# Kernel tuning notes

Measured on AMD Instinct MI355X. Metric: run time of the kernel, lower is better.

The kernel has to match this reference:

```python
import jax, jax.numpy as jnp
import numpy as np

HEADS = 8

def setup_inputs() -> dict:
    key = jax.random.key(0)
    k1, k2, k3, k4 = jax.random.split(key, 4)
    B, C_IN, H, W = 16, 256, 64, 64
    C_OUT = 256
    s = 1.0 / np.sqrt(C_IN)
    x = jax.random.normal(k1, (B, C_IN, H, W), dtype=jnp.float32)
    wq = jax.random.normal(k2, (C_OUT, C_IN), dtype=jnp.float32) * s
    wk = jax.random.normal(k3, (C_OUT, C_IN), dtype=jnp.float32) * s
    wv = jax.random.normal(k4, (C_OUT, C_IN), dtype=jnp.float32) * s
    return {"x": x, "wq": wq, "wk": wk, "wv": wv}

def _feat(t):
    # ELU(x) + 1  (positive feature map for linear attention)
    return jax.nn.elu(t) + 1.0

def reference(x, wq, wk, wv):
    B, C, H, W = x.shape
    M = H * W
    c_out = wq.shape[0]
    dh = c_out // HEADS
    scale = 1.0 / np.sqrt(dh)
    xf = x.reshape(B, C, M)  # flatten spatial
    # 1x1 conv (no bias) == channel matmul; reshape to [B, heads, dh, M]
    def proj(w):
        return jnp.einsum('oc,bcm->bom', w, xf).reshape(B, HEADS, dh, M)
    q = _feat(proj(wq)) * scale
    k = _feat(proj(wk)) * scale
    v = proj(wv)
    # linear attention: KV = k v^T over spatial, then apply to q
    KV = jnp.einsum('bhcm,bhdm->bhcd', k, v)          # [B,h,dh,dh]
    out = jnp.einsum('bhcd,bhcm->bhdm', KV, q)        # [B,h,dh,M]
    k_sum = k.sum(axis=-1)                             # [B,h,dh]
    denom = jnp.einsum('bhcm,bhc->bhm', q, k_sum)      # [B,h,M]
    denom = jnp.maximum(denom, 1e-6)[:, :, None, :]
    out = out / denom
    return out.reshape(B, c_out, H, W)
```

## Files before the change

### kernel.cpp

```cpp
#include <hip/hip_runtime.h>
#include <hip/hip_bf16.h>


typedef __attribute__((ext_vector_type(8))) short bf16x8;
typedef __attribute__((ext_vector_type(4))) float f32x4;
typedef __attribute__((ext_vector_type(4))) unsigned int u32x4;
typedef __attribute__((ext_vector_type(4))) float float4v;

#define DEVI static __device__ __forceinline__

DEVI unsigned short f2bf(float f){
  unsigned int u = __builtin_bit_cast(unsigned int, f);
  u = (u + 0x7fffu + ((u >> 16) & 1u)) >> 16;
  return (unsigned short)u;
}
DEVI unsigned int pk2(float a, float b){
  return (unsigned int)f2bf(a) | ((unsigned int)f2bf(b) << 16);
}
DEVI float feat(float p){
  return (p > 0.f ? p + 1.f : __expf(p)) * 0.17677669529663687f;
}

DEVI f32x4 mfma16(u32x4 a, u32x4 b, f32x4 c){
  return __builtin_amdgcn_mfma_f32_16x16x32_bf16(
      __builtin_bit_cast(bf16x8, a), __builtin_bit_cast(bf16x8, b), c, 0, 0, 0);
}

DEVI int swz8(int m){ return ((m ^ (m >> 3)) & 7) << 4; }

typedef __attribute__((address_space(3))) unsigned int as3_u32;
typedef __attribute__((address_space(1))) const unsigned int as1_u32;
DEVI void gload16(const void* g, void* l){
  __builtin_amdgcn_global_load_lds((as1_u32*)g, (as3_u32*)l, 16, 0, 0);
}
DEVI void stage_tile(const char* src, void* buf, int w, int lane){
  #pragma unroll
  for (int i = 0; i < 4; ++i){
    int ub = w * 1024 + i * 8192;
    gload16(src + ub + lane * 16, (char*)buf + ub);
  }
}

DEVI void stage_load(const float* __restrict__ xb, int m0, int tid, float4v* r){
  #pragma unroll
  for (int it = 0; it < 2; ++it){
    int cq = (tid >> 4) + it * 32;
    int mq = tid & 15;
    const float* p = xb + (size_t)(cq * 4) * 4096 + m0 + mq * 4;
    r[it*4+0] = *(const float4v*)(p);
    r[it*4+1] = *(const float4v*)(p + 4096);
    r[it*4+2] = *(const float4v*)(p + 8192);
    r[it*4+3] = *(const float4v*)(p + 12288);
  }
}
DEVI void stage_write(unsigned short* xT, int tid, const float4v* r){
  #pragma unroll
  for (int it = 0; it < 2; ++it){
    int cq = (tid >> 4) + it * 32;
    int mq = tid & 15;
    int c0 = cq * 4, ml0 = mq * 4;
    #pragma unroll
    for (int j = 0; j < 4; ++j){
      int m = ml0 + j;
      unsigned int lo = pk2(r[it*4+0][j], r[it*4+1][j]);
      unsigned int hi = pk2(r[it*4+2][j], r[it*4+3][j]);
      int off = m * 512 + ((c0 * 2) ^ swz8(m));
      unsigned long long v = (unsigned long long)lo | ((unsigned long long)hi << 32);
      *(unsigned long long*)((char*)xT + off) = v;
    }
  }
}
DEVI void dump_tile_sw(const unsigned short* xT, unsigned short* dst, int tid){
  #pragma unroll
  for (int i = 0; i < 4; ++i){
    int f = i * 512 + tid;
    int lane = f & 63, nt = (f >> 6) & 3, kk = f >> 8;
    int m = nt * 16 + (lane & 15);
    int col = (kk * 64 + (lane >> 4) * 16) ^ swz8(m);
    u32x4 v = *(const u32x4*)((const char*)xT + m * 512 + col);
    *(u32x4*)((char*)dst + (size_t)f * 16) = v;
  }
}

__global__ void wconv(const float* __restrict__ wq, const float* __restrict__ wk,
                      const float* __restrict__ wv,
                      unsigned short* __restrict__ wkvf, unsigned short* __restrict__ wqf){
  int t = blockIdx.x * 256 + threadIdx.x;
  if (t < 16384){
    int lane = t & 63, kk = (t >> 6) & 7, ot = (t >> 9) & 3, h = t >> 11;
    int l15 = lane & 15, hi = lane >> 4;
    const float* src = (ot < 2) ? (wk + (size_t)(h * 32 + ot * 16 + l15) * 256)
                                : (wv + (size_t)(h * 32 + (ot - 2) * 16 + l15) * 256);
    src += kk * 32 + hi * 8;
    unsigned short* dst = wkvf + (size_t)t * 8;
    #pragma unroll
    for (int j = 0; j < 8; ++j) dst[j] = f2bf(src[j]);
  } else if (t < 24576){
    int u = t - 16384;
    int lane = u & 63, kk = (u >> 6) & 7, ot = (u >> 9) & 1, h = u >> 10;
    int l15 = lane & 15, hi = lane >> 4;
    const float* src = wq + (size_t)(h * 32 + ot * 16 + l15) * 256 + kk * 32 + hi * 8;
    unsigned short* dst = wqf + (size_t)u * 8;
    #pragma unroll
    for (int j = 0; j < 8; ++j) dst[j] = f2bf(src[j]);
  }
}

DEVI void compute_sub_sw(const unsigned short* __restrict__ xT,
                         const unsigned short* __restrict__ wkvf,
                         int w, int l15, int hi, int lane,
                         f32x4 (&kvacc)[2][2], f32x4 (&ksacc)[2], u32x4 ones){
  #pragma unroll
  for (int g = 0; g < 2; ++g){
    f32x4 acc[2][4];
    #pragma unroll
    for (int a1 = 0; a1 < 2; ++a1)
      #pragma unroll
      for (int a2 = 0; a2 < 4; ++a2) acc[a1][a2] = f32x4{0.f,0.f,0.f,0.f};

    #pragma unroll
    for (int kk = 0; kk < 8; ++kk){
      u32x4 xf[2];
      #pragma unroll
      for (int n2 = 0; n2 < 2; ++n2){
        int m = (g * 2 + n2) * 16 + l15;
        xf[n2] = *(const u32x4*)((const char*)xT + m * 512 + ((kk * 64 + hi * 16) ^ swz8(m)));
      }
      #pragma unroll
      for (int ot = 0; ot < 4; ++ot){
        u32x4 wf = *(const u32x4*)(wkvf + ((((size_t)w * 4 + ot) * 8 + kk) * 64 + lane) * 8);
        #pragma unroll
        for (int n2 = 0; n2 < 2; ++n2) acc[n2][ot] = mfma16(xf[n2], wf, acc[n2][ot]);
      }
    }
    u32x4 kf[2], vf[2];
    #pragma unroll
    for (int t2 = 0; t2 < 2; ++t2){
      kf[t2][0] = pk2(feat(acc[0][t2][0]), feat(acc[0][t2][1]));
      kf[t2][1] = pk2(feat(acc[0][t2][2]), feat(acc[0][t2][3]));
      kf[t2][2] = pk2(feat(acc[1][t2][0]), feat(acc[1][t2][1]));
      kf[t2][3] = pk2(feat(acc[1][t2][2]), feat(acc[1][t2][3]));
      vf[t2][0] = pk2(acc[0][t2+2][0], acc[0][t2+2][1]);
      vf[t2][1] = pk2(acc[0][t2+2][2], acc[0][t2+2][3]);
      vf[t2][2] = pk2(acc[1][t2+2][0], acc[1][t2+2][1]);
      vf[t2][3] = pk2(acc[1][t2+2][2], acc[1][t2+2][3]);
    }
    #pragma unroll
    for (int ct = 0; ct < 2; ++ct){
      #pragma unroll
      for (int dt = 0; dt < 2; ++dt)
        kvacc[ct][dt] = mfma16(kf[ct], vf[dt], kvacc[ct][dt]);
      ksacc[ct] = mfma16(kf[ct], ones, ksacc[ct]);
    }
  }
}

__global__ void __launch_bounds__(512) xkv(const float* __restrict__ x,
        const unsigned short* __restrict__ wkvf,
        unsigned short* __restrict__ ximg,
        float* __restrict__ kvp, float* __restrict__ ksp){
  __shared__ __align__(16) unsigned short xT[16384];
  const int tid = threadIdx.x, lane = tid & 63, w = tid >> 6;
  const int l15 = lane & 15, hi = lane >> 4;
  const int t = blockIdx.x, b = blockIdx.y;
  const float* xb = x + (size_t)b * (256 * 4096);
  unsigned short* img = ximg + ((size_t)b * 64 + t) * 16384;

  f32x4 kvacc[2][2];
  f32x4 ksacc[2];
  #pragma unroll
  for (int i = 0; i < 2; ++i){
    ksacc[i] = f32x4{0.f,0.f,0.f,0.f};
    #pragma unroll
    for (int j = 0; j < 2; ++j) kvacc[i][j] = f32x4{0.f,0.f,0.f,0.f};
  }
  u32x4 ones = {0u,0u,0u,0u};
  if (l15 == 0){ ones[0] = ones[1] = ones[2] = ones[3] = 0x3f803f80u; }

  {
    float4v rs[8];
    stage_load(xb, t * 64, tid, rs);
    stage_write(xT, tid, rs);
  }
  __syncthreads();
  dump_tile_sw(xT, img, tid);
  compute_sub_sw(xT, wkvf, w, l15, hi, lane, kvacc, ksacc, ones);

  size_t base = (((size_t)b * 64 + t) * 8 + w) * 1024;
  #pragma unroll
  for (int ct = 0; ct < 2; ++ct){
    #pragma unroll
    for (int dt = 0; dt < 2; ++dt){
      #pragma unroll
      for (int r = 0; r < 4; ++r){
        int c = ct * 16 + hi * 4 + r, d = dt * 16 + l15;
        kvp[base + c * 32 + d] = kvacc[ct][dt][r];
      }
    }
  }
  if (l15 == 0){
    size_t kb = (((size_t)b * 64 + t) * 8 + w) * 32;
    #pragma unroll
    for (int ct = 0; ct < 2; ++ct)
      #pragma unroll
      for (int r = 0; r < 4; ++r) ksp[kb + ct * 16 + hi * 4 + r] = ksacc[ct][r];
  }
}

__global__ void k_red(const float* __restrict__ kvp, const float* __restrict__ ksp,
                      unsigned short* __restrict__ kvt, unsigned short* __restrict__ ksb){
  int t = blockIdx.x * 256 + threadIdx.x;
  int dq = t & 7;
  int c  = (t >> 3) & 31;
  int h  = (t >> 8) & 7;
  int b  = t >> 11;
  float4v s = {0.f,0.f,0.f,0.f};
  for (int c2 = 0; c2 < 64; ++c2){
    const float* p = kvp + ((((size_t)b * 64 + c2) * 8 + h) * 1024) + c * 32 + dq * 4;
    float4v r = *(const float4v*)p;
    s.x += r.x; s.y += r.y; s.z += r.z; s.w += r.w;
  }
  int pos = ((c >> 2) & 3) * 8 + ((c >> 4) << 2) + (c & 3);
  unsigned short* q = kvt + ((size_t)b * 8 + h) * 1024;
  q[(dq * 4 + 0) * 32 + pos] = f2bf(s.x);
  q[(dq * 4 + 1) * 32 + pos] = f2bf(s.y);
  q[(dq * 4 + 2) * 32 + pos] = f2bf(s.z);
  q[(dq * 4 + 3) * 32 + pos] = f2bf(s.w);
  if (dq == 0){
    float ks = 0.f;
    for (int c2 = 0; c2 < 64; ++c2)
      ks += ksp[(((size_t)b * 64 + c2) * 8 + h) * 32 + c];
    ksb[((size_t)b * 8 + h) * 32 + pos] = f2bf(ks);
  }
}

DEVI void q_sub(const unsigned short* __restrict__ xT,
                const unsigned short* __restrict__ wqf,
                u32x4 afkv0, u32x4 afkv1, u32x4 afd,
                int w, int l15, int hi, int lane, float* __restrict__ ob){
  f32x4 qa[2][4];
  #pragma unroll
  for (int a1 = 0; a1 < 2; ++a1)
    #pragma unroll
    for (int a2 = 0; a2 < 4; ++a2) qa[a1][a2] = f32x4{0.f,0.f,0.f,0.f};

  #pragma unroll
  for (int kk = 0; kk < 8; ++kk){
    u32x4 xf[4];
    #pragma unroll
    for (int nt = 0; nt < 4; ++nt)
      xf[nt] = *(const u32x4*)(xT + (((size_t)kk * 4 + nt) * 64 + lane) * 8);
    #pragma unroll
    for (int ot = 0; ot < 2; ++ot){
      u32x4 wf = *(const u32x4*)(wqf + ((((size_t)w * 2 + ot) * 8 + kk) * 64 + lane) * 8);
      #pragma unroll
      for (int nt = 0; nt < 4; ++nt) qa[ot][nt] = mfma16(wf, xf[nt], qa[ot][nt]);
    }
  }

  #pragma unroll
  for (int nt = 0; nt < 4; ++nt){
    u32x4 bq;
    bq[0] = pk2(feat(qa[0][nt][0]), feat(qa[0][nt][1]));
    bq[1] = pk2(feat(qa[0][nt][2]), feat(qa[0][nt][3]));
    bq[2] = pk2(feat(qa[1][nt][0]), feat(qa[1][nt][1]));
    bq[3] = pk2(feat(qa[1][nt][2]), feat(qa[1][nt][3]));

    f32x4 o0 = {0.f,0.f,0.f,0.f}, o1 = {0.f,0.f,0.f,0.f}, dn = {0.f,0.f,0.f,0.f};
    o0 = mfma16(afkv0, bq, o0);
    o1 = mfma16(afkv1, bq, o1);
    dn = mfma16(afd, bq, dn);
    float dv = __shfl(dn[0], l15, 64);
    float inv = 1.0f / fmaxf(dv, 1e-6f);
    #pragma unroll
    for (int r = 0; r < 4; ++r){
      ob[(size_t)(hi * 4 + r) * 4096 + nt * 16 + l15]      = o0[r] * inv;
      ob[(size_t)(16 + hi * 4 + r) * 4096 + nt * 16 + l15] = o1[r] * inv;
    }
  }
}

__global__ void __launch_bounds__(512) k_q(const unsigned short* __restrict__ ximg,
        const unsigned short* __restrict__ wqf,
        const unsigned short* __restrict__ kvt,
        const unsigned short* __restrict__ ksb,
        float* __restrict__ out){
  __shared__ __align__(16) unsigned short xT[2][16384];
  const int tid = threadIdx.x, lane = tid & 63, w = tid >> 6;
  const int l15 = lane & 15, hi = lane >> 4;
  const int ch = blockIdx.x, b = blockIdx.y;
  const char* src = (const char*)(ximg + ((size_t)b * 64 + ch * 2) * 16384);

  size_t kvbase = ((size_t)b * 8 + w) * 1024;
  u32x4 afkv0 = *(const u32x4*)(kvt + kvbase + (size_t)l15 * 32 + hi * 8);
  u32x4 afkv1 = *(const u32x4*)(kvt + kvbase + (size_t)(16 + l15) * 32 + hi * 8);
  u32x4 afd = {0u,0u,0u,0u};
  if (l15 == 0) afd = *(const u32x4*)(ksb + ((size_t)b * 8 + w) * 32 + hi * 8);

  stage_tile(src, xT[0], w, lane);
  __syncthreads();
  stage_tile(src + 32768, xT[1], w, lane);

  float* ob = out + ((size_t)b * 256 + w * 32) * 4096 + ch * 128;
  q_sub(xT[0], wqf, afkv0, afkv1, afd, w, l15, hi, lane, ob);
  __syncthreads();
  q_sub(xT[1], wqf, afkv0, afkv1, afd, w, l15, hi, lane, ob + 64);
}

extern "C" void kernel_launch(void* const* d_in, const int* in_sizes, int n_in,
                              void* d_out, int out_size, void* d_ws, size_t ws_size,
                              hipStream_t stream) {
  const float* x  = (const float*)d_in[0];
  const float* wq = (const float*)d_in[1];
  const float* wk = (const float*)d_in[2];
  const float* wv = (const float*)d_in[3];
  float* out = (float*)d_out;
  char* ws = (char*)d_ws;

  unsigned short* wkvf = (unsigned short*)(ws);
  unsigned short* wqf  = (unsigned short*)(ws + 262144);
  unsigned short* kvt  = (unsigned short*)(ws + 393216);
  unsigned short* ksb  = (unsigned short*)(ws + 655360);
  float* kvp = (float*)(ws + 1048576);
  float* ksp = (float*)(ws + 1048576 + 33554432);
  unsigned short* ximg = (unsigned short*)(ws + 1048576 + 33554432 + 1048576);

  hipLaunchKernelGGL(wconv, dim3(96), dim3(256), 0, stream, wq, wk, wv, wkvf, wqf);
  hipLaunchKernelGGL(xkv,   dim3(64, 16), dim3(512), 0, stream, x, wkvf, ximg, kvp, ksp);
  hipLaunchKernelGGL(k_red, dim3(128), dim3(256), 0, stream, kvp, ksp, kvt, ksb);
  hipLaunchKernelGGL(k_q,   dim3(32, 16), dim3(512), 0, stream, ximg, wqf, kvt, ksb, out);
}
```

Before: 80.07 us.

## Double-buffer x tiles in xkv with 1024-thread blocks over two chunks

The xkv kernel now runs 1024 threads per block, and each block handles two 64-column spatial tiles through a two-slot shared buffer. The global load of the second tile is issued before computing on the first, so memory latency can overlap with MFMA work. Each wave now handles one head and one 32-column half of a tile, and the partial-sum indexing is remapped to match. The manual bf16 rounding is also replaced with the library __float2bfloat16. The larger block raises per-block shared memory and register pressure under launch_bounds(1024), and the grid shrinks by half, which may lower occupancy.

```diff
diff --git a/kernel.cpp b/kernel.cpp
--- a/kernel.cpp
+++ b/kernel.cpp
@@ -10,9 +10,8 @@
 #define DEVI static __device__ __forceinline__
 
 DEVI unsigned short f2bf(float f){
-  unsigned int u = __builtin_bit_cast(unsigned int, f);
-  u = (u + 0x7fffu + ((u >> 16) & 1u)) >> 16;
-  return (unsigned short)u;
+  __hip_bfloat16 h = __float2bfloat16(f);
+  return __builtin_bit_cast(unsigned short, h);
 }
 DEVI unsigned int pk2(float a, float b){
   return (unsigned int)f2bf(a) | ((unsigned int)f2bf(b) << 16);
@@ -41,39 +40,33 @@
   }
 }
 
-DEVI void stage_load(const float* __restrict__ xb, int m0, int tid, float4v* r){
-  #pragma unroll
-  for (int it = 0; it < 2; ++it){
-    int cq = (tid >> 4) + it * 32;
-    int mq = tid & 15;
-    const float* p = xb + (size_t)(cq * 4) * 4096 + m0 + mq * 4;
-    r[it*4+0] = *(const float4v*)(p);
-    r[it*4+1] = *(const float4v*)(p + 4096);
-    r[it*4+2] = *(const float4v*)(p + 8192);
-    r[it*4+3] = *(const float4v*)(p + 12288);
-  }
-}
-DEVI void stage_write(unsigned short* xT, int tid, const float4v* r){
-  #pragma unroll
-  for (int it = 0; it < 2; ++it){
-    int cq = (tid >> 4) + it * 32;
-    int mq = tid & 15;
-    int c0 = cq * 4, ml0 = mq * 4;
-    #pragma unroll
-    for (int j = 0; j < 4; ++j){
-      int m = ml0 + j;
-      unsigned int lo = pk2(r[it*4+0][j], r[it*4+1][j]);
-      unsigned int hi = pk2(r[it*4+2][j], r[it*4+3][j]);
-      int off = m * 512 + ((c0 * 2) ^ swz8(m));
-      unsigned long long v = (unsigned long long)lo | ((unsigned long long)hi << 32);
-      *(unsigned long long*)((char*)xT + off) = v;
-    }
-  }
-}
-DEVI void dump_tile_sw(const unsigned short* xT, unsigned short* dst, int tid){
-  #pragma unroll
-  for (int i = 0; i < 4; ++i){
-    int f = i * 512 + tid;
+DEVI void stage_load1k(const float* __restrict__ xb, int m0, int tid, float4v* r){
+  int cq = tid >> 4;
+  int mq = tid & 15;
+  const float* p = xb + (size_t)(cq * 4) * 4096 + m0 + mq * 4;
+  r[0] = *(const float4v*)(p);
+  r[1] = *(const float4v*)(p + 4096);
+  r[2] = *(const float4v*)(p + 8192);
+  r[3] = *(const float4v*)(p + 12288);
+}
+DEVI void stage_write1k(unsigned short* xT, int tid, const float4v* r){
+  int cq = tid >> 4;
+  int mq = tid & 15;
+  int c0 = cq * 4, ml0 = mq * 4;
+  #pragma unroll
+  for (int j = 0; j < 4; ++j){
+    int m = ml0 + j;
+    unsigned int lo = pk2(r[0][j], r[1][j]);
+    unsigned int hi = pk2(r[2][j], r[3][j]);
+    int off = m * 512 + ((c0 * 2) ^ swz8(m));
+    unsigned long long v = (unsigned long long)lo | ((unsigned long long)hi << 32);
+    *(unsigned long long*)((char*)xT + off) = v;
+  }
+}
+DEVI void dump_tile_1k(const unsigned short* xT, unsigned short* dst, int tid){
+  #pragma unroll
+  for (int i = 0; i < 2; ++i){
+    int f = i * 1024 + tid;
     int lane = f & 63, nt = (f >> 6) & 3, kk = f >> 8;
     int m = nt * 16 + (lane & 15);
     int col = (kk * 64 + (lane >> 4) * 16) ^ swz8(m);
@@ -106,65 +99,63 @@
   }
 }
 
-DEVI void compute_sub_sw(const unsigned short* __restrict__ xT,
-                         const unsigned short* __restrict__ wkvf,
-                         int w, int l15, int hi, int lane,
-                         f32x4 (&kvacc)[2][2], f32x4 (&ksacc)[2], u32x4 ones){
-  #pragma unroll
-  for (int g = 0; g < 2; ++g){
-    f32x4 acc[2][4];
-    #pragma unroll
-    for (int a1 = 0; a1 < 2; ++a1)
+DEVI void compute_half_sw(const unsigned short* __restrict__ xT,
+                          const unsigned short* __restrict__ wkvf,
+                          int h, int g, int l15, int hi, int lane,
+                          f32x4 (&kvacc)[2][2], f32x4 (&ksacc)[2], u32x4 ones){
+  f32x4 acc[2][4];
+  #pragma unroll
+  for (int a1 = 0; a1 < 2; ++a1)
+    #pragma unroll
+    for (int a2 = 0; a2 < 4; ++a2) acc[a1][a2] = f32x4{0.f,0.f,0.f,0.f};
+
+  #pragma unroll
+  for (int kk = 0; kk < 8; ++kk){
+    u32x4 xf[2];
+    #pragma unroll
+    for (int n2 = 0; n2 < 2; ++n2){
+      int m = (g * 2 + n2) * 16 + l15;
+      xf[n2] = *(const u32x4*)((const char*)xT + m * 512 + ((kk * 64 + hi * 16) ^ swz8(m)));
+    }
+    #pragma unroll
+    for (int ot = 0; ot < 4; ++ot){
+      u32x4 wf = *(const u32x4*)(wkvf + ((((size_t)h * 4 + ot) * 8 + kk) * 64 + lane) * 8);
       #pragma unroll
-      for (int a2 = 0; a2 < 4; ++a2) acc[a1][a2] = f32x4{0.f,0.f,0.f,0.f};
-
-    #pragma unroll
-    for (int kk = 0; kk < 8; ++kk){
-      u32x4 xf[2];
-      #pragma unroll
-      for (int n2 = 0; n2 < 2; ++n2){
-        int m = (g * 2 + n2) * 16 + l15;
-        xf[n2] = *(const u32x4*)((const char*)xT + m * 512 + ((kk * 64 + hi * 16) ^ swz8(m)));
-      }
-      #pragma unroll
-      for (int ot = 0; ot < 4; ++ot){
-        u32x4 wf = *(const u32x4*)(wkvf + ((((size_t)w * 4 + ot) * 8 + kk) * 64 + lane) * 8);
-        #pragma unroll
-        for (int n2 = 0; n2 < 2; ++n2) acc[n2][ot] = mfma16(xf[n2], wf, acc[n2][ot]);
-      }
-    }
-    u32x4 kf[2], vf[2];
-    #pragma unroll
-    for (int t2 = 0; t2 < 2; ++t2){
-      kf[t2][0] = pk2(feat(acc[0][t2][0]), feat(acc[0][t2][1]));
-      kf[t2][1] = pk2(feat(acc[0][t2][2]), feat(acc[0][t2][3]));
-      kf[t2][2] = pk2(feat(acc[1][t2][0]), feat(acc[1][t2][1]));
-      kf[t2][3] = pk2(feat(acc[1][t2][2]), feat(acc[1][t2][3]));
-      vf[t2][0] = pk2(acc[0][t2+2][0], acc[0][t2+2][1]);
-      vf[t2][1] = pk2(acc[0][t2+2][2], acc[0][t2+2][3]);
-      vf[t2][2] = pk2(acc[1][t2+2][0], acc[1][t2+2][1]);
-      vf[t2][3] = pk2(acc[1][t2+2][2], acc[1][t2+2][3]);
-    }
-    #pragma unroll
-    for (int ct = 0; ct < 2; ++ct){
-      #pragma unroll
-      for (int dt = 0; dt < 2; ++dt)
-        kvacc[ct][dt] = mfma16(kf[ct], vf[dt], kvacc[ct][dt]);
-      ksacc[ct] = mfma16(kf[ct], ones, ksacc[ct]);
-    }
-  }
-}
-
-__global__ void __launch_bounds__(512) xkv(const float* __restrict__ x,
+      for (int n2 = 0; n2 < 2; ++n2) acc[n2][ot] = mfma16(xf[n2], wf, acc[n2][ot]);
+    }
+  }
+  u32x4 kf[2], vf[2];
+  #pragma unroll
+  for (int t2 = 0; t2 < 2; ++t2){
+    kf[t2][0] = pk2(feat(acc[0][t2][0]), feat(acc[0][t2][1]));
+    kf[t2][1] = pk2(feat(acc[0][t2][2]), feat(acc[0][t2][3]));
+    kf[t2][2] = pk2(feat(acc[1][t2][0]), feat(acc[1][t2][1]));
+    kf[t2][3] = pk2(feat(acc[1][t2][2]), feat(acc[1][t2][3]));
+    vf[t2][0] = pk2(acc[0][t2+2][0], acc[0][t2+2][1]);
+    vf[t2][1] = pk2(acc[0][t2+2][2], acc[0][t2+2][3]);
+    vf[t2][2] = pk2(acc[1][t2+2][0], acc[1][t2+2][1]);
+    vf[t2][3] = pk2(acc[1][t2+2][2], acc[1][t2+2][3]);
+  }
+  #pragma unroll
+  for (int ct = 0; ct < 2; ++ct){
+    #pragma unroll
+    for (int dt = 0; dt < 2; ++dt)
+      kvacc[ct][dt] = mfma16(kf[ct], vf[dt], kvacc[ct][dt]);
+    ksacc[ct] = mfma16(kf[ct], ones, ksacc[ct]);
+  }
+}
+
+__global__ void __launch_bounds__(1024) xkv(const float* __restrict__ x,
         const unsigned short* __restrict__ wkvf,
         unsigned short* __restrict__ ximg,
         float* __restrict__ kvp, float* __restrict__ ksp){
-  __shared__ __align__(16) unsigned short xT[16384];
+  __shared__ __align__(16) unsigned short xT[2][16384];
   const int tid = threadIdx.x, lane = tid & 63, w = tid >> 6;
   const int l15 = lane & 15, hi = lane >> 4;
-  const int t = blockIdx.x, b = blockIdx.y;
+  const int h = w >> 1, half = w & 1;
+  const int ch = blockIdx.x, b = blockIdx.y;
   const float* xb = x + (size_t)b * (256 * 4096);
-  unsigned short* img = ximg + ((size_t)b * 64 + t) * 16384;
+  unsigned short* img = ximg + ((size_t)b * 64 + ch * 2) * 16384;
 
   f32x4 kvacc[2][2];
   f32x4 ksacc[2];
@@ -177,16 +168,19 @@
   u32x4 ones = {0u,0u,0u,0u};
   if (l15 == 0){ ones[0] = ones[1] = ones[2] = ones[3] = 0x3f803f80u; }
 
-  {
-    float4v rs[8];
-    stage_load(xb, t * 64, tid, rs);
-    stage_write(xT, tid, rs);
-  }
+  float4v rs[4];
+  stage_load1k(xb, ch * 128, tid, rs);
+  stage_write1k(xT[0], tid, rs);
   __syncthreads();
-  dump_tile_sw(xT, img, tid);
-  compute_sub_sw(xT, wkvf, w, l15, hi, lane, kvacc, ksacc, ones);
-
-  size_t base = (((size_t)b * 64 + t) * 8 + w) * 1024;
+  stage_load1k(xb, ch * 128 + 64, tid, rs);
+  compute_half_sw(xT[0], wkvf, h, half, l15, hi, lane, kvacc, ksacc, ones);
+  dump_tile_1k(xT[0], img, tid);
+  stage_write1k(xT[1], tid, rs);
+  __syncthreads();
+  compute_half_sw(xT[1], wkvf, h, half, l15, hi, lane, kvacc, ksacc, ones);
+  dump_tile_1k(xT[1], img + 16384, tid);
+
+  size_t base = (((size_t)b * 64 + ch * 2 + half) * 8 + h) * 1024;
   #pragma unroll
   for (int ct = 0; ct < 2; ++ct){
     #pragma unroll
@@ -199,7 +193,7 @@
     }
   }
   if (l15 == 0){
-    size_t kb = (((size_t)b * 64 + t) * 8 + w) * 32;
+    size_t kb = (((size_t)b * 64 + ch * 2 + half) * 8 + h) * 32;
     #pragma unroll
     for (int ct = 0; ct < 2; ++ct)
       #pragma unroll
@@ -326,7 +320,7 @@
   unsigned short* ximg = (unsigned short*)(ws + 1048576 + 33554432 + 1048576);
 
   hipLaunchKernelGGL(wconv, dim3(96), dim3(256), 0, stream, wq, wk, wv, wkvf, wqf);
-  hipLaunchKernelGGL(xkv,   dim3(64, 16), dim3(512), 0, stream, x, wkvf, ximg, kvp, ksp);
+  hipLaunchKernelGGL(xkv,   dim3(32, 16), dim3(1024), 0, stream, x, wkvf, ximg, kvp, ksp);
   hipLaunchKernelGGL(k_red, dim3(128), dim3(256), 0, stream, kvp, ksp, kvt, ksb);
   hipLaunchKernelGGL(k_q,   dim3(32, 16), dim3(512), 0, stream, ximg, wqf, kvt, ksb, out);
 }
```

Result: slower. 84.16 us (+5.1%).
